# Kernel tuning notes

Measured on AMD Instinct MI355X. Metric: run time of the kernel, lower is better.

Reference implementation:

```python
import jax, jax.numpy as jnp
import numpy as np

N_CELLS = 131072
IN_DIM = 128
HID = 256
OUT = 128
MLP = 128          # hardcoded 128-wide MLP inside BenchMind
N_FACTIONS = 8
SYNC = 0.15
DEBATE = 0.15


def setup_inputs() -> dict:
    key = jax.random.key(0)
    ks = jax.random.split(key, 20)
    s = 0.05
    d = {}
    d['x'] = jax.random.normal(ks[0], (1, IN_DIM), jnp.float32)
    d['payoffs'] = jax.random.uniform(ks[1], (N_CELLS,), jnp.float32) * 5.0
    d['last_action'] = jax.random.randint(ks[2], (N_CELLS,), 0, 2, dtype=jnp.int32)
    d['step'] = 10
    d['hiddens'] = jax.random.normal(ks[3], (N_CELLS, HID), jnp.float32) * 0.1
    d['a_w1'] = jax.random.normal(ks[4], (MLP, IN_DIM + HID), jnp.float32) * s
    d['a_b1'] = jax.random.normal(ks[5], (MLP,), jnp.float32) * s
    d['a_w2'] = jax.random.normal(ks[6], (OUT, MLP), jnp.float32) * s
    d['a_b2'] = jax.random.normal(ks[7], (OUT,), jnp.float32) * s
    d['g_w1'] = jax.random.normal(ks[8], (MLP, IN_DIM + HID), jnp.float32) * s
    d['g_b1'] = jax.random.normal(ks[9], (MLP,), jnp.float32) * s
    d['g_w2'] = jax.random.normal(ks[10], (OUT, MLP), jnp.float32) * s
    d['g_b2'] = jax.random.normal(ks[11], (OUT,), jnp.float32) * s
    d['gru_wih'] = jax.random.normal(ks[12], (3 * HID, OUT + 1), jnp.float32) * s
    d['gru_whh'] = jax.random.normal(ks[13], (3 * HID, HID), jnp.float32) * s
    d['gru_bih'] = jax.random.normal(ks[14], (3 * HID,), jnp.float32) * s
    d['gru_bhh'] = jax.random.normal(ks[15], (3 * HID,), jnp.float32) * s
    d['head_w'] = jax.random.normal(ks[16], (IN_DIM, OUT), jnp.float32) * s
    d['head_b'] = jax.random.normal(ks[17], (IN_DIM,), jnp.float32) * s
    return d


def reference(x, payoffs, last_action, step, hiddens,
              a_w1, a_b1, a_w2, a_b2, g_w1, g_b1, g_w2, g_b2,
              gru_wih, gru_whh, gru_bih, gru_bhh, head_w, head_b):
    n = hiddens.shape[0]
    # ---- batched BenchMind.forward over all cells (same x broadcast) ----
    xb = jnp.broadcast_to(x, (n, x.shape[-1]))
    comb = jnp.concatenate([xb, hiddens], axis=-1)               # (N, IN+HID)
    a = jnp.maximum(comb @ a_w1.T + a_b1, 0.0) @ a_w2.T + a_b2   # (N, OUT)
    g = jnp.maximum(comb @ g_w1.T + g_b1, 0.0) @ g_w2.T + g_b2
    out = a - g                                                  # (N, OUT)
    tension = jnp.mean(out * out, axis=-1)                       # (N,)
    # detached GRU input (output.detach(), tension.detach())
    mem_in = jax.lax.stop_gradient(
        jnp.concatenate([out, tension[:, None]], axis=-1))       # (N, OUT+1)
    # torch GRUCell math
    gi = mem_in @ gru_wih.T + gru_bih                            # (N, 3H)
    gh = hiddens @ gru_whh.T + gru_bhh
    i_r, i_z, i_n = jnp.split(gi, 3, axis=-1)
    h_r, h_z, h_n = jnp.split(gh, 3, axis=-1)
    r = jax.nn.sigmoid(i_r + h_r)
    z = jax.nn.sigmoid(i_z + h_z)
    nn_ = jnp.tanh(i_n + r * h_n)
    new_h = (1.0 - z) * nn_ + z * hiddens                        # (N, HID)
    # ---- payoff modulation + clamp ----
    payoff_scale = payoffs[:, None] / 5.0
    new_h = jnp.clip(new_h * (0.9 + 0.1 * payoff_scale), -10.0, 10.0)
    new_h = jax.lax.stop_gradient(new_h)                         # hiddens detached
    # ---- faction_sync_debate ----
    fs = n // N_FACTIONS
    h3 = new_h.reshape(N_FACTIONS, fs, HID)
    h3 = (1.0 - SYNC) * h3 + SYNC * h3.mean(axis=1, keepdims=True)
    if step > 5:  # step is a Python int
        global_op = h3.mean(axis=1).mean(axis=0)                 # (HID,)
        dc = max(1, fs // 4)
        h3 = h3.at[:, :dc].set((1.0 - DEBATE) * h3[:, :dc] + DEBATE * global_op)
    h2 = h3.reshape(n, HID)
    # ---- cooperators pull to mean, defectors get noise ----
    coop = last_action.astype(h2.dtype)[:, None]
    gmean = h2.mean(axis=0, keepdims=True)
    h2 = h2 + 0.05 * coop * (gmean - h2)
    noise = jax.random.normal(jax.random.key(42), h2.shape, h2.dtype)
    h2 = h2 + 0.02 * (1.0 - coop) * noise
    new_hiddens = jnp.clip(h2, -10.0, 10.0)
    # ---- tension-softmax mixture of cell outputs (weights detached: .item()) ----
    w = jax.lax.stop_gradient(jax.nn.softmax(tension))           # (N,)
    combined = w @ out                                           # (OUT,)
    pred = (combined @ head_w.T + head_b)[None, :]               # (1, IN_DIM)
    avg_tension = tension.mean()
    return pred, avg_tension, new_hiddens
```

## Files before the change

### kernel.cpp

```cpp
#include <hip/hip_runtime.h>

#define NCELLS 131072
#define HIDN 256
#define ODIM 128
#define FS 16384
#define DCC 4096
#define HALF_NOISE 16777216u

#define WS_WAG   0u
#define WS_W2C   131072u
#define WS_WIH   196608u
#define WS_WHH   393216u
#define WS_BAG   786432u
#define WS_B2C   787456u
#define WS_ACC   788480u
#define ACC_F     (WS_ACC/4)
#define ACC_BYTES 17152u
#define WS_FM    805632u
#define WS_GOP   813824u
#define WS_GMEAN 814848u

typedef __bf16 bf16x8 __attribute__((ext_vector_type(8)));
typedef float floatx4 __attribute__((ext_vector_type(4)));
#define MFMA16(a,b,c) __builtin_amdgcn_mfma_f32_16x16x32_bf16((a),(b),(c),0,0,0)

__device__ __forceinline__ unsigned short f2bf(float f){
  union { float f; unsigned int u; } v; v.f = f;
  unsigned int u = v.u;
  unsigned int r = (u + 0x7FFFu + ((u >> 16) & 1u)) >> 16;
  return (unsigned short)r;
}
__device__ __forceinline__ float bf2f(unsigned short s){
  union { unsigned int u; float f; } v; v.u = ((unsigned int)s) << 16; return v.f;
}
__device__ __forceinline__ float sigm(float x){ return 1.0f/(1.0f + expf(-x)); }

__device__ __forceinline__ bf16x8 ldfrag(const unsigned short* base, int row, int chunk, int width){
  return *(const bf16x8*)(base + row*width + (((chunk ^ (row & 7))) << 3));
}

__device__ __forceinline__ unsigned int rotl32(unsigned int x, int r){ return (x<<r)|(x>>(32-r)); }
__device__ __forceinline__ void threefry_0_42(unsigned int x0, unsigned int x1,
                                              unsigned int& o0, unsigned int& o1){
  const unsigned int k0 = 0u, k1 = 42u, k2 = 0x1BD11BDAu ^ 0u ^ 42u;
  x0 += k0; x1 += k1;
#define TFR(r) { x0 += x1; x1 = rotl32(x1,(r)); x1 ^= x0; }
  TFR(13) TFR(15) TFR(26) TFR(6)
  x0 += k1; x1 += k2 + 1u;
  TFR(17) TFR(29) TFR(16) TFR(24)
  x0 += k2; x1 += k0 + 2u;
  TFR(13) TFR(15) TFR(26) TFR(6)
  x0 += k0; x1 += k1 + 3u;
  TFR(17) TFR(29) TFR(16) TFR(24)
  x0 += k1; x1 += k2 + 4u;
  TFR(13) TFR(15) TFR(26) TFR(6)
  x0 += k2; x1 += k0 + 5u;
#undef TFR
  o0 = x0; o1 = x1;
}

__device__ __forceinline__ unsigned int tf_bits_partitionable(unsigned int idx){
  unsigned int o0, o1;
  threefry_0_42(0u, idx, o0, o1);
  return o0 ^ o1;
}

__device__ __forceinline__ float giles_erfinv(float x){
  float w = -log1pf(-x*x);
  float p;
  if (w < 5.0f){
    w = w - 2.5f;
    p = 2.81022636e-08f;
    p = 3.43273939e-07f + p*w;
    p = -3.5233877e-06f + p*w;
    p = -4.39150654e-06f + p*w;
    p = 0.00021858087f  + p*w;
    p = -0.00125372503f + p*w;
    p = -0.00417768164f + p*w;
    p = 0.246640727f    + p*w;
    p = 1.50140941f     + p*w;
  } else {
    w = sqrtf(w) - 3.0f;
    p = -0.000200214257f;
    p = 0.000100950558f + p*w;
    p = 0.00134934322f  + p*w;
    p = -0.00367342844f + p*w;
    p = 0.00573950773f  + p*w;
    p = -0.0076224613f  + p*w;
    p = 0.00943887047f  + p*w;
    p = 1.00167406f     + p*w;
    p = 2.83297682f     + p*w;
  }
  return p*x;
}
__device__ __forceinline__ float bits_to_normal(unsigned int bits){
  union { unsigned int u; float f; } v; v.u = (bits >> 9) | 0x3f800000u;
  float f = v.f - 1.0f;
  const float lo = -0.99999994f;
  float u = fmaf(f, 2.0f, lo);
  u = fmaxf(u, lo);
  return 1.41421356237f * giles_erfinv(u);
}

__global__ void k_prep_w(const float* a_w1, const float* g_w1, const float* a_w2, const float* g_w2,
                         const float* gru_wih, const float* gru_whh, unsigned short* ws16){
  int i = blockIdx.x*256 + threadIdx.x;
  if (i < 65536){
    int ch = i >> 8, k = i & 255;
    float v = (ch < 128) ? a_w1[ch*384 + 128 + k] : g_w1[(ch-128)*384 + 128 + k];
    ws16[WS_WAG/2 + i] = f2bf(v);
  } else if (i < 98304){
    int j = i - 65536; int ch = j >> 8, k = j & 255;
    float v = (k < 128) ? a_w2[ch*128 + k] : -g_w2[ch*128 + (k-128)];
    ws16[WS_W2C/2 + j] = f2bf(v);
  } else if (i < 196608){
    int j = i - 98304; int ch = j >> 7, k = j & 127;
    ws16[WS_WIH/2 + j] = f2bf(gru_wih[ch*129 + k]);
  } else if (i < 393216){
    int j = i - 196608; int ch = j >> 8, k = j & 255;
    ws16[WS_WHH/2 + j] = f2bf(gru_whh[ch*256 + k]);
  }
}

__global__ void k_prep_b(const float* x, const float* a_w1, const float* g_w1,
                         const float* a_b1, const float* g_b1,
                         const float* a_b2, const float* g_b2, float* wsf){
  int t = threadIdx.x;
  const float* wr = (t < 128) ? (a_w1 + t*384) : (g_w1 + (t-128)*384);
  float b = (t < 128) ? a_b1[t] : g_b1[t-128];
  float s = 0.f;
  for (int k = 0; k < 128; ++k) s += x[k]*wr[k];
  wsf[WS_BAG/4 + t] = b + s;
  if (t < 128) wsf[WS_B2C/4 + t] = a_b2[t] - g_b2[t];
}

__device__ __forceinline__ void gemm_gi(floatx4 acc[4][2], const unsigned short* Wih,
                                        const unsigned short* outlds, int cb, int lane, int rowoff){
  const int al = lane & 15, kg = lane >> 4;
#pragma unroll
  for (int kk = 0; kk < 4; ++kk){
    const int chunk = kk*4 + kg;
    bf16x8 a0 = ldfrag(outlds,      al, chunk, 128);
    bf16x8 a1 = ldfrag(outlds, 16 + al, chunk, 128);
    bf16x8 a2 = ldfrag(outlds, 32 + al, chunk, 128);
    bf16x8 a3 = ldfrag(outlds, 48 + al, chunk, 128);
    const int k = kk*32 + kg*8;
    bf16x8 b0 = *(const bf16x8*)(Wih + (rowoff + cb      + al)*128 + k);
    bf16x8 b1 = *(const bf16x8*)(Wih + (rowoff + cb + 16 + al)*128 + k);
    acc[0][0] = MFMA16(a0,b0,acc[0][0]); acc[1][0] = MFMA16(a1,b0,acc[1][0]);
    acc[2][0] = MFMA16(a2,b0,acc[2][0]); acc[3][0] = MFMA16(a3,b0,acc[3][0]);
    acc[0][1] = MFMA16(a0,b1,acc[0][1]); acc[1][1] = MFMA16(a1,b1,acc[1][1]);
    acc[2][1] = MFMA16(a2,b1,acc[2][1]); acc[3][1] = MFMA16(a3,b1,acc[3][1]);
  }
}
__device__ __forceinline__ void gemm_gh(floatx4 acc[4][2], const unsigned short* Whh,
                                        const unsigned short* hlds, int cb, int lane, int rowoff){
  const int al = lane & 15, kg = lane >> 4;
#pragma unroll
  for (int kk = 0; kk < 8; ++kk){
    const int chunk = kk*4 + kg;
    bf16x8 a0 = ldfrag(hlds,      al, chunk, 256);
    bf16x8 a1 = ldfrag(hlds, 16 + al, chunk, 256);
    bf16x8 a2 = ldfrag(hlds, 32 + al, chunk, 256);
    bf16x8 a3 = ldfrag(hlds, 48 + al, chunk, 256);
    const int k = kk*32 + kg*8;
    bf16x8 b0 = *(const bf16x8*)(Whh + (rowoff + cb      + al)*256 + k);
    bf16x8 b1 = *(const bf16x8*)(Whh + (rowoff + cb + 16 + al)*256 + k);
    acc[0][0] = MFMA16(a0,b0,acc[0][0]); acc[1][0] = MFMA16(a1,b0,acc[1][0]);
    acc[2][0] = MFMA16(a2,b0,acc[2][0]); acc[3][0] = MFMA16(a3,b0,acc[3][0]);
    acc[0][1] = MFMA16(a0,b1,acc[0][1]); acc[1][1] = MFMA16(a1,b1,acc[1][1]);
    acc[2][1] = MFMA16(a2,b1,acc[2][1]); acc[3][1] = MFMA16(a3,b1,acc[3][1]);
  }
}

__global__ __launch_bounds__(512, 2) void k_pass1(
    const float* __restrict__ hiddens, const float* __restrict__ payoffs,
    const float* __restrict__ gru_wih, const float* __restrict__ gru_bih,
    const float* __restrict__ gru_bhh,
    const unsigned short* __restrict__ ws16, const float* __restrict__ wsf,
    float* __restrict__ accf, float* __restrict__ d_out)
{
  __shared__ __align__(16) unsigned short h_lds[64*256];
  __shared__ __align__(16) unsigned short u1[64*256];
  unsigned short* u2 = u1;
  float* tens = (float*)&u1[8192];
  float* texp = tens + 64;
  float* pay  = tens + 128;
  float* bsum = tens + 192;

  const int tid = threadIdx.x;
  const int lane = tid & 63;
  const int wid  = tid >> 6;
  const int row0 = blockIdx.x * 64;
  const int al = lane & 15, kg = lane >> 4;
  const floatx4 vzero = {0.f, 0.f, 0.f, 0.f};

  {
    const float4* hg = (const float4*)(hiddens + (size_t)row0*256);
#pragma unroll
    for (int it = 0; it < 8; ++it){
      int i = it*512 + tid;
      float4 v = hg[i];
      int row = i >> 6;
      int ch  = (i & 63) << 2;
      int off = row*256 + (((ch >> 3) ^ (row & 7)) << 3) + (ch & 7);
      h_lds[off+0] = f2bf(v.x); h_lds[off+1] = f2bf(v.y);
      h_lds[off+2] = f2bf(v.z); h_lds[off+3] = f2bf(v.w);
    }
  }
  __syncthreads();

  {
    const unsigned short* Wag = ws16 + WS_WAG/2;
    const int mrow = (wid >> 2) * 32;
    const int ncol = (wid & 3) * 64;
    floatx4 acc[2][4];
#pragma unroll
    for (int m=0;m<2;m++)
#pragma unroll
      for (int n=0;n<4;n++) acc[m][n] = vzero;
#pragma unroll
    for (int kk = 0; kk < 8; ++kk){
      const int chunk = kk*4 + kg;
      bf16x8 a0 = ldfrag(h_lds, mrow      + al, chunk, 256);
      bf16x8 a1 = ldfrag(h_lds, mrow + 16 + al, chunk, 256);
      const int k = kk*32 + kg*8;
      bf16x8 b0 = *(const bf16x8*)(Wag + (ncol      + al)*256 + k);
      bf16x8 b1 = *(const bf16x8*)(Wag + (ncol + 16 + al)*256 + k);
      bf16x8 b2 = *(const bf16x8*)(Wag + (ncol + 32 + al)*256 + k);
      bf16x8 b3 = *(const bf16x8*)(Wag + (ncol + 48 + al)*256 + k);
      acc[0][0] = MFMA16(a0,b0,acc[0][0]); acc[1][0] = MFMA16(a1,b0,acc[1][0]);
      acc[0][1] = MFMA16(a0,b1,acc[0][1]); acc[1][1] = MFMA16(a1,b1,acc[1][1]);
      acc[0][2] = MFMA16(a0,b2,acc[0][2]); acc[1][2] = MFMA16(a1,b2,acc[1][2]);
      acc[0][3] = MFMA16(a0,b3,acc[0][3]); acc[1][3] = MFMA16(a1,b3,acc[1][3]);
    }
#pragma unroll
    for (int n=0;n<4;n++){
      int ch = ncol + n*16 + al;
      float bias = wsf[WS_BAG/4 + ch];
#pragma unroll
      for (int m=0;m<2;m++){
#pragma unroll
        for (int r=0;r<4;r++){
          int row = mrow + m*16 + kg*4 + r;
          float val = fmaxf(acc[m][n][r] + bias, 0.f);
          u1[row*256 + (((ch>>3) ^ (row&7))<<3) + (ch&7)] = f2bf(val);
        }
      }
    }
  }
  __syncthreads();

  floatx4 bacc[2][2];
  const int bmrow = (wid >> 2) * 32;
  const int bncol = (wid & 3) * 32;
  {
    const unsigned short* W2c = ws16 + WS_W2C/2;
#pragma unroll
    for (int m=0;m<2;m++)
#pragma unroll
      for (int n=0;n<2;n++) bacc[m][n] = vzero;
#pragma unroll
    for (int kk = 0; kk < 8; ++kk){
      const int chunk = kk*4 + kg;
      bf16x8 a0 = ldfrag(u1, bmrow      + al, chunk, 256);
      bf16x8 a1 = ldfrag(u1, bmrow + 16 + al, chunk, 256);
      const int k = kk*32 + kg*8;
      bf16x8 b0 = *(const bf16x8*)(W2c + (bncol      + al)*256 + k);
      bf16x8 b1 = *(const bf16x8*)(W2c + (bncol + 16 + al)*256 + k);
      bacc[0][0] = MFMA16(a0,b0,bacc[0][0]); bacc[1][0] = MFMA16(a1,b0,bacc[1][0]);
      bacc[0][1] = MFMA16(a0,b1,bacc[0][1]); bacc[1][1] = MFMA16(a1,b1,bacc[1][1]);
    }
  }
  __syncthreads();
  {
#pragma unroll
    for (int n=0;n<2;n++){
      int ch = bncol + n*16 + al;
      float bias = wsf[WS_B2C/4 + ch];
#pragma unroll
      for (int m=0;m<2;m++){
#pragma unroll
        for (int r=0;r<4;r++){
          int row = bmrow + m*16 + kg*4 + r;
          u2[row*128 + (((ch>>3) ^ (row&7))<<3) + (ch&7)] = f2bf(bacc[m][n][r] + bias);
        }
      }
    }
  }
  __syncthreads();

  if (tid < 256){
    int row = tid >> 2, part = tid & 3;
    float s = 0.f;
    for (int c = 0; c < 32; ++c){
      int ch = part*32 + c;
      float o = bf2f(u2[row*128 + (((ch>>3) ^ (row&7))<<3) + (ch&7)]);
      s += o*o;
    }
    bsum[tid] = s;
  }
  __syncthreads();
  if (tid < 64){
    float t = (bsum[tid*4] + bsum[tid*4+1] + bsum[tid*4+2] + bsum[tid*4+3]) * (1.0f/128.0f);
    tens[tid] = t;
    texp[tid] = expf(t);
    pay[tid]  = payoffs[row0 + tid];
  }
  __syncthreads();

  if (tid < 128){
    int ch = tid;
    float s = 0.f;
    for (int row = 0; row < 64; ++row)
      s += texp[row] * bf2f(u2[row*128 + (((ch>>3) ^ (row&7))<<3) + (ch&7)]);
    atomicAdd(accf + ACC_F + 4096 + ch, s);
  } else if (tid == 128){
    float se = 0.f, st = 0.f;
    for (int r = 0; r < 64; ++r){ se += texp[r]; st += tens[r]; }
    atomicAdd(accf + ACC_F + 4224, se);
    atomicAdd(accf + ACC_F + 4225, st);
  }

  const unsigned short* Wih = ws16 + WS_WIH/2;
  const unsigned short* Whh = ws16 + WS_WHH/2;
  const int cb = wid * 32;

  float rr[4][2][4];
  {
    floatx4 acc[4][2];
#pragma unroll
    for (int m=0;m<4;m++){ acc[m][0] = vzero; acc[m][1] = vzero; }
    gemm_gi(acc, Wih, u2, cb, lane, 0);
    gemm_gh(acc, Whh, h_lds, cb, lane, 0);
#pragma unroll
    for (int n=0;n<2;n++){
      int ch = cb + n*16 + al;
      float bb = gru_bih[ch] + gru_bhh[ch];
      float wt = gru_wih[ch*129 + 128];
#pragma unroll
      for (int m=0;m<4;m++)
#pragma unroll
        for (int r=0;r<4;r++){
          int row = m*16 + kg*4 + r;
          rr[m][n][r] = sigm(acc[m][n][r] + bb + tens[row]*wt);
        }
    }
  }

  float nnv[4][2][4];
  {
    floatx4 gin[4][2], ghn[4][2];
#pragma unroll
    for (int m=0;m<4;m++){ gin[m][0]=vzero; gin[m][1]=vzero; ghn[m][0]=vzero; ghn[m][1]=vzero; }
    gemm_gi(gin, Wih, u2, cb, lane, 512);
    gemm_gh(ghn, Whh, h_lds, cb, lane, 512);
#pragma unroll
    for (int n=0;n<2;n++){
      int ch = cb + n*16 + al;
      float bi = gru_bih[512+ch];
      float bh = gru_bhh[512+ch];
      float wt = gru_wih[(512+ch)*129 + 128];
#pragma unroll
      for (int m=0;m<4;m++)
#pragma unroll
        for (int r=0;r<4;r++){
          int row = m*16 + kg*4 + r;
          nnv[m][n][r] = tanhf(gin[m][n][r] + bi + tens[row]*wt + rr[m][n][r]*(ghn[m][n][r] + bh));
        }
    }
  }

  {
    floatx4 acc[4][2];
#pragma unroll
    for (int m=0;m<4;m++){ acc[m][0] = vzero; acc[m][1] = vzero; }
    gemm_gi(acc, Wih, u2, cb, lane, 256);
    gemm_gh(acc, Whh, h_lds, cb, lane, 256);
    float cs[2] = {0.f, 0.f};
#pragma unroll
    for (int n=0;n<2;n++){
      int ch = cb + n*16 + al;
      float bb = gru_bih[256+ch] + gru_bhh[256+ch];
      float wt = gru_wih[(256+ch)*129 + 128];
#pragma unroll
      for (int m=0;m<4;m++)
#pragma unroll
        for (int r=0;r<4;r++){
          int row = m*16 + kg*4 + r;
          float z = sigm(acc[m][n][r] + bb + tens[row]*wt);
          float h = bf2f(h_lds[row*256 + (((ch>>3) ^ (row&7))<<3) + (ch&7)]);
          float nh = (1.0f - z)*nnv[m][n][r] + z*h;
          nh *= (0.9f + 0.02f*pay[row]);
          nh = fminf(fmaxf(nh, -10.0f), 10.0f);
          d_out[129 + (size_t)(row0 + row)*256 + ch] = nh;
          cs[n] += nh;
        }
    }
#pragma unroll
    for (int n=0;n<2;n++){
      float c = cs[n];
      c += __shfl_xor(c, 16);
      c += __shfl_xor(c, 32);
      if (lane < 16) bsum[cb + n*16 + lane] = c;
    }
  }
  __syncthreads();

  if (tid < 256){
    int f = row0 >> 14;
    atomicAdd(accf + ACC_F + f*256 + tid, bsum[tid]);
    if ((row0 & (FS-1)) < DCC)
      atomicAdd(accf + ACC_F + 2048 + f*256 + tid, bsum[tid]);
  }
}

__global__ void k_mid(const float* __restrict__ accf, float* __restrict__ wsf,
                      const float* __restrict__ head_w, const float* __restrict__ head_b,
                      const int* __restrict__ stepp, float* __restrict__ d_out){
  int t = threadIdx.x;
  const float* fsum   = accf + ACC_F;
  const float* fsumdc = fsum + 2048;
  const float* comb   = fsum + 4096;
  int step = *stepp;

  float g = 0.f;
  for (int f = 0; f < 8; ++f) g += fsum[f*256 + t];
  float gop = g * (1.0f/131072.0f);
  wsf[WS_GOP/4 + t] = gop;

  float tot = 0.f;
  for (int f = 0; f < 8; ++f){
    float s1  = fsum[f*256 + t];
    float fmv = s1 * (1.0f/16384.0f);
    wsf[WS_FM/4 + f*256 + t] = fmv;
    float sh2 = s1;
    if (step > 5){
      float sdc = 0.85f*fsumdc[f*256 + t] + 0.15f*4096.0f*fmv;
      sh2 = s1 + 0.15f*(4096.0f*gop - sdc);
    }
    tot += sh2;
  }
  wsf[WS_GMEAN/4 + t] = tot * (1.0f/131072.0f);

  if (t < 128){
    float inv = 1.0f / fsum[4224];
    float p = head_b[t];
    for (int ch = 0; ch < 128; ++ch) p += head_w[t*128 + ch] * (comb[ch]*inv);
    d_out[t] = p;
  }
  if (t == 0) d_out[128] = fsum[4225] * (1.0f/131072.0f);
}

__global__ __launch_bounds__(256) void k_pass2(float* __restrict__ dout,
                                               const int* __restrict__ last_action,
                                               const float* __restrict__ wsf,
                                               const int* __restrict__ stepp){
  const int t = threadIdx.x;
  const int rA = blockIdx.x*8 + (t >> 5);
  const int rB = rA + 65536;
  const int ch0 = (t & 31) * 8;
  const int step = *stepp;
  const float* fm    = wsf + WS_FM/4;
  const float* gop   = wsf + WS_GOP/4;
  const float* gmean = wsf + WS_GMEAN/4;
  const int coopA = last_action[rA];
  const int coopB = last_action[rB];
  const bool debA = (step > 5) && ((rA & (FS-1)) < DCC);
  const bool debB = (step > 5) && ((rB & (FS-1)) < DCC);
  const int fA = rA >> 14, fB = rB >> 14;
  float* pa = dout + 129 + (size_t)rA*256 + ch0;
  float* pb = dout + 129 + (size_t)rB*256 + ch0;

  float va[8], vb[8];
#pragma unroll
  for (int i=0;i<8;i++){ va[i] = pa[i]; vb[i] = pb[i]; }
#pragma unroll
  for (int i=0;i<8;i++){
    int ch = ch0 + i;
    float p = 0.85f*va[i] + 0.15f*fm[fA*256 + ch];
    if (debA) p = 0.85f*p + 0.15f*gop[ch];
    if (coopA) p += 0.05f*(gmean[ch] - p);
    va[i] = p;
    float q = 0.85f*vb[i] + 0.15f*fm[fB*256 + ch];
    if (debB) q = 0.85f*q + 0.15f*gop[ch];
    if (coopB) q += 0.05f*(gmean[ch] - q);
    vb[i] = q;
  }
  if (!coopA){
    const unsigned baseA = (unsigned)rA*256u + (unsigned)ch0;
#pragma unroll
    for (int i=0;i<8;i++)
      va[i] += 0.02f*bits_to_normal(tf_bits_partitionable(baseA + i));
  }
  if (!coopB){
    const unsigned baseB = (unsigned)rA*256u + (unsigned)ch0 + HALF_NOISE;
#pragma unroll
    for (int i=0;i<8;i++)
      vb[i] += 0.02f*bits_to_normal(tf_bits_partitionable(baseB + i));
  }
#pragma unroll
  for (int i=0;i<8;i++){
    pa[i] = fminf(fmaxf(va[i], -10.f), 10.f);
    pb[i] = fminf(fmaxf(vb[i], -10.f), 10.f);
  }
}

extern "C" void kernel_launch(void* const* d_in, const int* in_sizes, int n_in,
                              void* d_out, int out_size, void* d_ws, size_t ws_size,
                              hipStream_t stream){
  (void)in_sizes; (void)n_in; (void)out_size; (void)ws_size;
  const float* x          = (const float*)d_in[0];
  const float* payoffs    = (const float*)d_in[1];
  const int*   last_action= (const int*)d_in[2];
  const int*   step       = (const int*)d_in[3];
  const float* hiddens    = (const float*)d_in[4];
  const float* a_w1       = (const float*)d_in[5];
  const float* a_b1       = (const float*)d_in[6];
  const float* a_w2       = (const float*)d_in[7];
  const float* a_b2       = (const float*)d_in[8];
  const float* g_w1       = (const float*)d_in[9];
  const float* g_b1       = (const float*)d_in[10];
  const float* g_w2       = (const float*)d_in[11];
  const float* g_b2       = (const float*)d_in[12];
  const float* gru_wih    = (const float*)d_in[13];
  const float* gru_whh    = (const float*)d_in[14];
  const float* gru_bih    = (const float*)d_in[15];
  const float* gru_bhh    = (const float*)d_in[16];
  const float* head_w     = (const float*)d_in[17];
  const float* head_b     = (const float*)d_in[18];

  unsigned short* ws16 = (unsigned short*)d_ws;
  float* wsf = (float*)d_ws;
  float* outp = (float*)d_out;

  hipMemsetAsync((char*)d_ws + WS_ACC, 0, ACC_BYTES, stream);
  k_prep_w<<<1536, 256, 0, stream>>>(a_w1, g_w1, a_w2, g_w2, gru_wih, gru_whh, ws16);
  k_prep_b<<<1, 256, 0, stream>>>(x, a_w1, g_w1, a_b1, g_b1, a_b2, g_b2, wsf);
  k_pass1<<<2048, 512, 0, stream>>>(hiddens, payoffs, gru_wih, gru_bih, gru_bhh,
                                    ws16, wsf, wsf, outp);
  k_mid<<<1, 256, 0, stream>>>(wsf, wsf, head_w, head_b, step, outp);
  k_pass2<<<8192, 256, 0, stream>>>(outp, last_action, wsf, step);
}
```

Before: 758.8 us.

## Fuse bias prep into weight prep, use fast math, and compute tension in registers

Merges the single-block bias-prep kernel into the weight-prep launch as an extra block, removing one kernel launch. Replaces expf/tanhf with fast exp and hardware reciprocal approximations in the GRU gates. Packs the bf16 LDS stores of hiddens into 64-bit writes. Computes the per-row squared-sum tension from fp32 accumulators with wave shuffles instead of re-reading bf16 values from LDS, which removes a barrier. Vectorizes the head matvec. Fast math changes numerics slightly, and tension now comes from fp32 rather than bf16-rounded values.

Result: faster. 711.8 us (-6.2%).

```diff
diff --git a/kernel.cpp b/kernel.cpp
--- a/kernel.cpp
+++ b/kernel.cpp
@@ -33,7 +33,12 @@
 __device__ __forceinline__ float bf2f(unsigned short s){
   union { unsigned int u; float f; } v; v.u = ((unsigned int)s) << 16; return v.f;
 }
-__device__ __forceinline__ float sigm(float x){ return 1.0f/(1.0f + expf(-x)); }
+__device__ __forceinline__ float sigm(float x){
+  return __builtin_amdgcn_rcpf(1.0f + __expf(-x));
+}
+__device__ __forceinline__ float ftanh(float x){
+  return 1.0f - 2.0f*__builtin_amdgcn_rcpf(1.0f + __expf(2.0f*x));
+}
 
 __device__ __forceinline__ bf16x8 ldfrag(const unsigned short* base, int row, int chunk, int width){
   return *(const bf16x8*)(base + row*width + (((chunk ^ (row & 7))) << 3));
@@ -103,7 +108,25 @@
 }
 
 __global__ void k_prep_w(const float* a_w1, const float* g_w1, const float* a_w2, const float* g_w2,
-                         const float* gru_wih, const float* gru_whh, unsigned short* ws16){
+                         const float* gru_wih, const float* gru_whh, unsigned short* ws16,
+                         const float* x, const float* a_b1, const float* g_b1,
+                         const float* a_b2, const float* g_b2, float* wsf){
+  if (blockIdx.x == 1536){
+    int t = threadIdx.x;
+    const float* wr = (t < 128) ? (a_w1 + t*384) : (g_w1 + (t-128)*384);
+    float b = (t < 128) ? a_b1[t] : g_b1[t-128];
+    const float4* wr4 = (const float4*)wr;
+    const float4* x4  = (const float4*)x;
+    float s = 0.f;
+#pragma unroll 4
+    for (int k = 0; k < 32; ++k){
+      float4 w = wr4[k], xv = x4[k];
+      s += w.x*xv.x + w.y*xv.y + w.z*xv.z + w.w*xv.w;
+    }
+    wsf[WS_BAG/4 + t] = b + s;
+    if (t < 128) wsf[WS_B2C/4 + t] = a_b2[t] - g_b2[t];
+    return;
+  }
   int i = blockIdx.x*256 + threadIdx.x;
   if (i < 65536){
     int ch = i >> 8, k = i & 255;
@@ -122,18 +145,6 @@
   }
 }
 
-__global__ void k_prep_b(const float* x, const float* a_w1, const float* g_w1,
-                         const float* a_b1, const float* g_b1,
-                         const float* a_b2, const float* g_b2, float* wsf){
-  int t = threadIdx.x;
-  const float* wr = (t < 128) ? (a_w1 + t*384) : (g_w1 + (t-128)*384);
-  float b = (t < 128) ? a_b1[t] : g_b1[t-128];
-  float s = 0.f;
-  for (int k = 0; k < 128; ++k) s += x[k]*wr[k];
-  wsf[WS_BAG/4 + t] = b + s;
-  if (t < 128) wsf[WS_B2C/4 + t] = a_b2[t] - g_b2[t];
-}
-
 __device__ __forceinline__ void gemm_gi(floatx4 acc[4][2], const unsigned short* Wih,
                                         const unsigned short* outlds, int cb, int lane, int rowoff){
   const int al = lane & 15, kg = lane >> 4;
@@ -204,8 +215,9 @@
       int row = i >> 6;
       int ch  = (i & 63) << 2;
       int off = row*256 + (((ch >> 3) ^ (row & 7)) << 3) + (ch & 7);
-      h_lds[off+0] = f2bf(v.x); h_lds[off+1] = f2bf(v.y);
-      h_lds[off+2] = f2bf(v.z); h_lds[off+3] = f2bf(v.w);
+      unsigned int p0 = (unsigned int)f2bf(v.x) | ((unsigned int)f2bf(v.y) << 16);
+      unsigned int p1 = (unsigned int)f2bf(v.z) | ((unsigned int)f2bf(v.w) << 16);
+      *(uint2*)(h_lds + off) = make_uint2(p0, p1);
     }
   }
   __syncthreads();
@@ -273,7 +285,13 @@
     }
   }
   __syncthreads();
-  {
+
+  {
+    float ts[2][4];
+#pragma unroll
+    for (int m=0;m<2;m++)
+#pragma unroll
+      for (int r=0;r<4;r++) ts[m][r] = 0.f;
 #pragma unroll
     for (int n=0;n<2;n++){
       int ch = bncol + n*16 + al;
@@ -283,28 +301,29 @@
 #pragma unroll
         for (int r=0;r<4;r++){
           int row = bmrow + m*16 + kg*4 + r;
-          u2[row*128 + (((ch>>3) ^ (row&7))<<3) + (ch&7)] = f2bf(bacc[m][n][r] + bias);
+          float val = bacc[m][n][r] + bias;
+          u2[row*128 + (((ch>>3) ^ (row&7))<<3) + (ch&7)] = f2bf(val);
+          ts[m][r] += val*val;
         }
       }
     }
-  }
-  __syncthreads();
-
-  if (tid < 256){
-    int row = tid >> 2, part = tid & 3;
-    float s = 0.f;
-    for (int c = 0; c < 32; ++c){
-      int ch = part*32 + c;
-      float o = bf2f(u2[row*128 + (((ch>>3) ^ (row&7))<<3) + (ch&7)]);
-      s += o*o;
-    }
-    bsum[tid] = s;
+#pragma unroll
+    for (int m=0;m<2;m++)
+#pragma unroll
+      for (int r=0;r<4;r++){
+        float s = ts[m][r];
+        s += __shfl_xor(s, 1);
+        s += __shfl_xor(s, 2);
+        s += __shfl_xor(s, 4);
+        s += __shfl_xor(s, 8);
+        if (al == 0) bsum[(bmrow + m*16 + kg*4 + r)*4 + (wid & 3)] = s;
+      }
   }
   __syncthreads();
   if (tid < 64){
     float t = (bsum[tid*4] + bsum[tid*4+1] + bsum[tid*4+2] + bsum[tid*4+3]) * (1.0f/128.0f);
     tens[tid] = t;
-    texp[tid] = expf(t);
+    texp[tid] = __expf(t);
     pay[tid]  = payoffs[row0 + tid];
   }
   __syncthreads();
@@ -366,7 +385,7 @@
 #pragma unroll
         for (int r=0;r<4;r++){
           int row = m*16 + kg*4 + r;
-          nnv[m][n][r] = tanhf(gin[m][n][r] + bi + tens[row]*wt + rr[m][n][r]*(ghn[m][n][r] + bh));
+          nnv[m][n][r] = ftanh(gin[m][n][r] + bi + tens[row]*wt + rr[m][n][r]*(ghn[m][n][r] + bh));
         }
     }
   }
@@ -445,9 +464,14 @@
 
   if (t < 128){
     float inv = 1.0f / fsum[4224];
-    float p = head_b[t];
-    for (int ch = 0; ch < 128; ++ch) p += head_w[t*128 + ch] * (comb[ch]*inv);
-    d_out[t] = p;
+    const float4* hw = (const float4*)(head_w + t*128);
+    const float4* cb4 = (const float4*)comb;
+    float p = 0.f;
+    for (int c = 0; c < 32; ++c){
+      float4 w = hw[c], cc = cb4[c];
+      p += w.x*cc.x + w.y*cc.y + w.z*cc.z + w.w*cc.w;
+    }
+    d_out[t] = head_b[t] + p*inv;
   }
   if (t == 0) d_out[128] = fsum[4225] * (1.0f/131072.0f);
 }
@@ -535,8 +559,8 @@
   float* outp = (float*)d_out;
 
   hipMemsetAsync((char*)d_ws + WS_ACC, 0, ACC_BYTES, stream);
-  k_prep_w<<<1536, 256, 0, stream>>>(a_w1, g_w1, a_w2, g_w2, gru_wih, gru_whh, ws16);
-  k_prep_b<<<1, 256, 0, stream>>>(x, a_w1, g_w1, a_b1, g_b1, a_b2, g_b2, wsf);
+  k_prep_w<<<1537, 256, 0, stream>>>(a_w1, g_w1, a_w2, g_w2, gru_wih, gru_whh, ws16,
+                                     x, a_b1, g_b1, a_b2, g_b2, wsf);
   k_pass1<<<2048, 512, 0, stream>>>(hiddens, payoffs, gru_wih, gru_bih, gru_bhh,
                                     ws16, wsf, wsf, outp);
   k_mid<<<1, 256, 0, stream>>>(wsf, wsf, head_w, head_b, step, outp);
```
